# Optimization experiments

Hardware: AMD Instinct MI355X
Metric: run time of the kernel (lower is better)

Reference implementation:

```python
import jax, jax.numpy as jnp
import numpy as np

B, N, M, D = 128, 256, 8, 768  # batch, input patches, memory tokens, embed dim


def setup_inputs() -> dict:
    key = jax.random.key(0)
    ks = jax.random.split(key, 6)
    w_scale = D ** -0.5
    return {
        "x": jax.random.normal(ks[0], (B, N, D), dtype=jnp.float32),
        "memory": jax.random.normal(ks[1], (M, D), dtype=jnp.float32) * 0.02,
        "Wq": jax.random.normal(ks[2], (D, D), dtype=jnp.float32) * w_scale,
        "bq": jnp.zeros((D,), dtype=jnp.float32),
        "Wk": jax.random.normal(ks[3], (D, D), dtype=jnp.float32) * w_scale,
        "bk": jnp.zeros((D,), dtype=jnp.float32),
        "Wv": jax.random.normal(ks[4], (D, D), dtype=jnp.float32) * w_scale,
        "bv": jnp.zeros((D,), dtype=jnp.float32),
        "Wo": jax.random.normal(ks[5], (D, D), dtype=jnp.float32) * w_scale,
        "bo": jnp.zeros((D,), dtype=jnp.float32),
    }


def reference(x, memory, Wq, bq, Wk, bk, Wv, bv, Wo, bo):
    b, n, d = x.shape
    m = memory.shape[0]
    t = n + m
    scaling = d ** -0.5  # mha.scaling = 1/sqrt(input_dim)
    # concat input patches with expanded memory tokens: [B, T, D]
    cat = jnp.concatenate([x, jnp.broadcast_to(memory[None], (b, m, d))], axis=1)
    q = cat @ Wq + bq
    k = cat @ Wk + bk
    v = cat @ Wv + bv
    # full attention matrix [B, T, T], softmax over keys
    att = jax.nn.softmax(jnp.einsum("bqd,bkd->bqk", q, k) * scaling, axis=-1)
    # post-softmax multiplicative mask: zero all rows for memory-token queries
    row_mask = (jnp.arange(t) < n).astype(att.dtype)[None, :, None]  # [1, T, 1]
    att = att * row_mask
    head_out = jnp.einsum("bqk,bkd->bqd", att, v)
    attended = head_out @ Wo + bo
    # return only the input-patch part (split(...)[0])
    return attended[:, :n, :]
```

## Files before the change

kernel.cpp:

```cpp
#include <hip/hip_runtime.h>
#include <hip/hip_bf16.h>

typedef __attribute__((ext_vector_type(4))) float f32x4;
typedef __attribute__((ext_vector_type(8))) short short8;
typedef __attribute__((ext_vector_type(4))) unsigned short us4;
typedef unsigned short u16;

#define DEVI __device__ __forceinline__

#define BB 128
#define NN 256
#define MMEM 8
#define DD 768
#define TT 264
#define TP 320
#define SP 384
#define AROWS2 33024

DEVI u16 f2bf(float f) {
  __hip_bfloat16 b = __float2bfloat16(f);
  u16 u; __builtin_memcpy(&u, &b, 2); return u;
}

DEVI float bf2f(u16 u) {
  unsigned int v = ((unsigned int)u) << 16;
  float f; __builtin_memcpy(&f, &v, 4); return f;
}

DEVI void gload_lds16(const void* g, void* l) {
  __builtin_amdgcn_global_load_lds((const __attribute__((address_space(1))) void*)g,
                                   (__attribute__((address_space(3))) void*)l, 16, 0, 0);
}


__global__ __launch_bounds__(256)
void conv_x(const float* __restrict__ x, const float* __restrict__ mem, u16* __restrict__ Ab) {
  const long total4 = (long)AROWS2 * DD / 4;
  for (long i = (long)blockIdx.x * blockDim.x + threadIdx.x; i < total4;
       i += (long)gridDim.x * blockDim.x) {
    long e = i * 4;
    int row = (int)(e / DD);
    int cb  = (int)(e % DD);
    f32x4 v = {0.f, 0.f, 0.f, 0.f};
    if (row < BB * NN)             v = *(const f32x4*)(x   + (size_t)row * DD + cb);
    else if (row < BB * NN + MMEM) v = *(const f32x4*)(mem + (size_t)(row - BB * NN) * DD + cb);
    us4 o = {f2bf(v[0]), f2bf(v[1]), f2bf(v[2]), f2bf(v[3])};
    *(us4*)(Ab + e) = o;
  }
}

__global__ __launch_bounds__(256)
void conv_w(const float* __restrict__ Wq, const float* __restrict__ Wk,
            const float* __restrict__ Wv, const float* __restrict__ Wo,
            u16* __restrict__ Wqt, u16* __restrict__ Wkt,
            u16* __restrict__ Wvt, u16* __restrict__ Wot) {
  const int total = 4 * DD * DD;
  for (int i = blockIdx.x * blockDim.x + threadIdx.x; i < total;
       i += gridDim.x * blockDim.x) {
    int mat = i / (DD * DD), rem = i % (DD * DD);
    int j = rem / DD, d = rem % DD;
    const float* W = (mat == 0) ? Wq : (mat == 1) ? Wk : (mat == 2) ? Wv : Wo;
    u16* Wt = (mat == 0) ? Wqt : (mat == 1) ? Wkt : (mat == 2) ? Wvt : Wot;
    Wt[(size_t)j * DD + d] = f2bf(W[(size_t)d * DD + j]);
  }
}


#define BAR()    __builtin_amdgcn_s_barrier()
#define CFENCE() asm volatile("" ::: "memory")
#define VM2()    asm volatile("s_waitcnt vmcnt(2)" ::: "memory")
#define VMW0()   asm volatile("s_waitcnt vmcnt(0)" ::: "memory")

#define STG(gb, ld, isB, ss, rg, kt) do {                                       \
    const u16* _s = (gb) + (size_t)((rg) * 16 + srow) * (ld) + (kt) * 64 + scol;\
    char* _d = smem + (ss) * 65536 + (isB) * 32768 + (rg) * 2048;               \
    gload_lds16(_s, _d);                                                        \
    gload_lds16(_s + 32, _d + 1024);                                            \
  } while (0)

#define STG_A0(ss, kt) STG(Ab, LDA, 0, ss, ((w & 3) | ((w & 4) << 1)), kt)
#define STG_B0(ss, kt) STG(Bb, LDB, 1, ss, ((w & 1) | ((w & 6) << 1)), kt)
#define STG_A1(ss, kt) STG(Ab, LDA, 0, ss, (((w & 3) | ((w & 4) << 1)) + 4), kt)
#define STG_B1(ss, kt) STG(Bb, LDB, 1, ss, (((w & 1) | ((w & 6) << 1)) + 2), kt)

#define RD_A(dst, s, QM)                                                          \
  _Pragma("unroll") for (int mi = 0; mi < 4; ++mi)                                \
  _Pragma("unroll") for (int ks = 0; ks < 2; ++ks)                                \
    dst[mi][ks] = *(const short8*)(smem + (s) * 65536 +                           \
                    ((wm * 8 + (QM) * 4 + mi) * 2 + ks) * 1024 + fbase);

#define RD_B(dst, s, QN)                                                          \
  _Pragma("unroll") for (int ni = 0; ni < 2; ++ni)                                \
  _Pragma("unroll") for (int ks = 0; ks < 2; ++ks)                                \
    dst[ni][ks] = *(const short8*)(smem + (s) * 65536 + 32768 +                   \
                    ((wn * 4 + (QN) * 2 + ni) * 2 + ks) * 1024 + fbase);

#define MM(FA, FB, QM, QN)                                                        \
  _Pragma("unroll") for (int mi = 0; mi < 4; ++mi)                                \
  _Pragma("unroll") for (int ni = 0; ni < 2; ++ni)                                \
  _Pragma("unroll") for (int ks = 0; ks < 2; ++ks)                                \
    acc[(QM)*4+mi][(QN)*2+ni] = __builtin_amdgcn_mfma_f32_16x16x32_bf16(          \
        FA[mi][ks], FB[ni][ks], acc[(QM)*4+mi][(QN)*2+ni], 0, 0, 0);

template<int MODE>
__global__ __launch_bounds__(512)
void gemm256(const u16* __restrict__ A, const u16* __restrict__ Bq,
             const u16* __restrict__ Bk, const u16* __restrict__ Bv,
             const float* __restrict__ b0, const float* __restrict__ b1,
             const float* __restrict__ b2,
             u16* __restrict__ Oq, u16* __restrict__ Ok, u16* __restrict__ Ov,
             float* __restrict__ FO, int NT)
{
  extern __shared__ char smem[];
  const int tid = threadIdx.x;
  const int l = tid & 63;
  const int w = tid >> 6;
  const int wm = w >> 2, wn = w & 3;

  constexpr int LDA = (MODE == 2) ? TP : DD;
  constexpr int LDB = (MODE == 2) ? TP : DD;

  const int nwg = gridDim.x * gridDim.y;
  const int lin = blockIdx.y * gridDim.x + blockIdx.x;
  const int qq = nwg >> 3, rr = nwg & 7;
  const int xcd = lin & 7, idx = lin >> 3;
  const int wg = (xcd < rr ? xcd * (qq + 1) : rr * (qq + 1) + (xcd - rr) * qq) + idx;
  const int tn = wg % gridDim.x;
  const int tmz = wg / gridDim.x;

  const u16* Ab; const u16* Bb;
  int matsel = 0;
  if constexpr (MODE == 0) {
    Ab = A + (size_t)tmz * 256 * DD;
    matsel = tn / 3;
    const u16* Wp = (matsel == 0) ? Bq : (matsel == 1) ? Bk : Bv;
    Bb = Wp + (size_t)(tn % 3) * 256 * DD;
  } else if constexpr (MODE == 1) {
    Ab = A + (size_t)tmz * 256 * DD;
    Bb = Bq + (size_t)tn * 256 * DD;
  } else {
    Ab = A + (size_t)tmz * NN * TP;
    Bb = Bq + ((size_t)tmz * DD + tn * 256) * TP;
  }

  const int jj = (l < 32) ? l : (l ^ 2);
  const int srow = jj >> 2;
  const int scol = (jj & 3) * 8;
  const int fbase = (((l & 15) * 64) + ((l >> 4) * 16)) ^ (((l >> 3) & 1) << 5);

  f32x4 acc[8][4];
  #pragma unroll
  for (int i = 0; i < 8; ++i)
    #pragma unroll
    for (int jx = 0; jx < 4; ++jx) acc[i][jx] = (f32x4){0.f, 0.f, 0.f, 0.f};

  short8 fa0[4][2], fa1[4][2], fb0[2][2], fb1[2][2];

  STG_A0(0, 0); STG_B0(0, 0); STG_A1(0, 0); STG_B1(0, 0);
  VMW0(); BAR(); CFENCE();
  RD_A(fa0, 0, 0); RD_B(fb0, 0, 0);

  for (int g = 0; g < NT; ++g) {
    const int s = g & 1, ss = s ^ 1;
    const int st = (g + 1 < NT) ? (g + 1) : (NT - 1);

    VM2(); BAR(); CFENCE();
    RD_A(fa1, s, 1);
    STG_A0(ss, st);
    __builtin_amdgcn_s_setprio(1); MM(fa0, fb0, 0, 0); __builtin_amdgcn_s_setprio(0);

    VM2(); BAR(); CFENCE();
    RD_B(fb1, s, 1);
    STG_B0(ss, st);
    __builtin_amdgcn_s_setprio(1); MM(fa1, fb0, 1, 0); __builtin_amdgcn_s_setprio(0);

    STG_A1(ss, st);
    __builtin_amdgcn_s_setprio(1); MM(fa0, fb1, 0, 1); __builtin_amdgcn_s_setprio(0);

    VM2(); BAR(); CFENCE();
    RD_A(fa0, ss, 0); RD_B(fb0, ss, 0);
    STG_B1(ss, st);
    __builtin_amdgcn_s_setprio(1); MM(fa1, fb1, 1, 1); __builtin_amdgcn_s_setprio(0);
  }

  const int fr = l & 15, fro = (l >> 4) * 4;
  if constexpr (MODE == 0) {
    const float* bias = (matsel == 0) ? b0 : (matsel == 1) ? b1 : b2;
    u16* ob = (matsel == 0) ? Oq : (matsel == 1) ? Ok : Ov;
    const int cb = (tn % 3) * 256 + wn * 64;
    const size_t rb = (size_t)tmz * 256 + wm * 128;
    #pragma unroll
    for (int MI = 0; MI < 8; ++MI)
      #pragma unroll
      for (int NI = 0; NI < 4; ++NI) {
        const int col = cb + NI * 16 + fr;
        const float bvv = bias[col];
        #pragma unroll
        for (int r = 0; r < 4; ++r)
          ob[(rb + MI * 16 + fro + r) * DD + col] = f2bf(acc[MI][NI][r] + bvv);
      }
  } else if constexpr (MODE == 1) {
    const int cb = tn * 256 + wn * 64;
    const size_t rb = (size_t)tmz * 256 + wm * 128;
    #pragma unroll
    for (int MI = 0; MI < 8; ++MI)
      #pragma unroll
      for (int NI = 0; NI < 4; ++NI) {
        const int col = cb + NI * 16 + fr;
        const float bvv = b0[col];
        #pragma unroll
        for (int r = 0; r < 4; ++r)
          FO[(rb + MI * 16 + fro + r) * DD + col] = acc[MI][NI][r] + bvv;
      }
  } else {
    const int cb = tn * 256 + wn * 64;
    const size_t rb = (size_t)tmz * NN + wm * 128;
    #pragma unroll
    for (int MI = 0; MI < 8; ++MI)
      #pragma unroll
      for (int NI = 0; NI < 4; ++NI) {
        const int col = cb + NI * 16 + fr;
        #pragma unroll
        for (int r = 0; r < 4; ++r)
          Oq[(rb + MI * 16 + fro + r) * DD + col] = f2bf(acc[MI][NI][r]);
      }
  }
}


__global__ __launch_bounds__(256)
void gemm_s(const u16* __restrict__ A, const u16* __restrict__ Bm,
            u16* __restrict__ F0)
{
  const int tid = threadIdx.x;
  const int l  = tid & 63;
  const int w  = tid >> 6;
  const int wm = w >> 1, wn = w & 1;
  const int tm = blockIdx.x, tn = blockIdx.y, z = blockIdx.z;

  __shared__ u16 lsA[128 * 32];
  __shared__ u16 lsB[128 * 32];

  const u16* Abase = A + ((size_t)z * NN + tm * 128) * DD;

  f32x4 acc[4][4];
  #pragma unroll
  for (int i = 0; i < 4; i++)
    #pragma unroll
    for (int j = 0; j < 4; j++) acc[i][j] = (f32x4){0.f, 0.f, 0.f, 0.f};

  const int srow = l >> 2;
  const int scol = (l & 3) * 8;

  for (int kt = 0; kt < 24; ++kt) {
    const int kpos = kt * 32 + scol;
    #pragma unroll
    for (int q = 0; q < 2; ++q) {
      const int r = q * 64 + w * 16 + srow;
      gload_lds16(Abase + (size_t)r * DD + kpos, &lsA[q * 2048 + w * 512]);
    }
    #pragma unroll
    for (int q = 0; q < 2; ++q) {
      const int r = q * 64 + w * 16 + srow;
      const int t = tn * 128 + r;
      const int rr = (t < NN) ? (z * NN + t)
                   : ((t < TT) ? (BB * NN + t - NN) : BB * NN);
      gload_lds16(Bm + (size_t)rr * DD + kpos, &lsB[q * 2048 + w * 512]);
    }
    __syncthreads();

    const int fr = l & 15, fk = (l >> 4) * 8;
    short8 fa[4], fb[4];
    #pragma unroll
    for (int mi = 0; mi < 4; mi++)
      fa[mi] = *(const short8*)&lsA[(wm * 64 + mi * 16 + fr) * 32 + fk];
    #pragma unroll
    for (int ni = 0; ni < 4; ni++)
      fb[ni] = *(const short8*)&lsB[(wn * 64 + ni * 16 + fr) * 32 + fk];
    #pragma unroll
    for (int mi = 0; mi < 4; mi++)
      #pragma unroll
      for (int ni = 0; ni < 4; ni++)
        acc[mi][ni] = __builtin_amdgcn_mfma_f32_16x16x32_bf16(fa[mi], fb[ni], acc[mi][ni], 0, 0, 0);
    __syncthreads();
  }

  const int fr  = l & 15;
  const int fro = (l >> 4) * 4;
  const float scl = 0.03608439182435161f;
  u16* Sb = F0 + (size_t)z * NN * SP;
  const int cb = tn * 128 + wn * 64;
  const int rb = tm * 128 + wm * 64;
  #pragma unroll
  for (int mi = 0; mi < 4; mi++)
    #pragma unroll
    for (int ni = 0; ni < 4; ni++)
      #pragma unroll
      for (int r = 0; r < 4; r++)
        Sb[(size_t)(rb + mi * 16 + fro + r) * SP + cb + ni * 16 + fr] = f2bf(acc[mi][ni][r] * scl);
}


__global__ __launch_bounds__(256)
void softmax_k(const u16* __restrict__ S, u16* __restrict__ P) {
  const int l = threadIdx.x & 63;
  const int row = blockIdx.x * 4 + (threadIdx.x >> 6);
  const u16* s = S + (size_t)row * SP;
  float v0 = bf2f(s[l]), v1 = bf2f(s[64 + l]), v2 = bf2f(s[128 + l]), v3 = bf2f(s[192 + l]);
  float v4 = (l < 8) ? bf2f(s[256 + l]) : -__builtin_inff();
  float m = fmaxf(fmaxf(fmaxf(v0, v1), fmaxf(v2, v3)), v4);
  #pragma unroll
  for (int off = 32; off; off >>= 1) m = fmaxf(m, __shfl_xor(m, off));
  float e0 = __expf(v0 - m), e1 = __expf(v1 - m), e2 = __expf(v2 - m), e3 = __expf(v3 - m);
  float e4 = (l < 8) ? __expf(v4 - m) : 0.f;
  float sum = e0 + e1 + e2 + e3 + e4;
  #pragma unroll
  for (int off = 32; off; off >>= 1) sum += __shfl_xor(sum, off);
  const float inv = 1.f / sum;
  u16* p = P + (size_t)row * TP;
  p[l] = f2bf(e0 * inv); p[64 + l] = f2bf(e1 * inv);
  p[128 + l] = f2bf(e2 * inv); p[192 + l] = f2bf(e3 * inv);
  if (l < 8) p[256 + l] = f2bf(e4 * inv);
  else       p[256 + l] = 0;
}


__global__ __launch_bounds__(256)
void transpose_v(const u16* __restrict__ V, u16* __restrict__ Vt) {
  __shared__ u16 ls[64 * 66];
  const int b = blockIdx.z;
  const int d0 = blockIdx.x * 64;
  const int t0 = blockIdx.y * 64;
  const int tid = threadIdx.x;
  #pragma unroll
  for (int q = 0; q < 2; ++q) {
    const int idx = q * 256 + tid;
    const int tr = idx >> 3;
    const int dg = (idx & 7) * 8;
    const int t = t0 + tr;
    short8 v = (short8)(short)0;
    if (t < NN)       v = *(const short8*)(V + ((size_t)b * NN + t) * DD + d0 + dg);
    else if (t < TT)  v = *(const short8*)(V + (size_t)(BB * NN + t - NN) * DD + d0 + dg);
    #pragma unroll
    for (int e = 0; e < 8; ++e) ls[tr * 66 + dg + e] = (u16)v[e];
  }
  __syncthreads();
  #pragma unroll
  for (int q = 0; q < 2; ++q) {
    const int idx = q * 256 + tid;
    const int dr = idx >> 3;
    const int tg = (idx & 7) * 8;
    short8 v;
    #pragma unroll
    for (int e = 0; e < 8; ++e) v[e] = (short)ls[(tg + e) * 66 + dr];
    *(short8*)(Vt + ((size_t)b * DD + d0 + dr) * TP + t0 + tg) = v;
  }
}


extern "C" void kernel_launch(void* const* d_in, const int* in_sizes, int n_in,
                              void* d_out, int out_size, void* d_ws, size_t ws_size,
                              hipStream_t stream) {
  const float* x   = (const float*)d_in[0];
  const float* mem = (const float*)d_in[1];
  const float* Wq  = (const float*)d_in[2];
  const float* bq  = (const float*)d_in[3];
  const float* Wk  = (const float*)d_in[4];
  const float* bk  = (const float*)d_in[5];
  const float* Wv  = (const float*)d_in[6];
  const float* bv  = (const float*)d_in[7];
  const float* Wo  = (const float*)d_in[8];
  const float* bo  = (const float*)d_in[9];
  float* out = (float*)d_out;
  (void)ws_size; (void)in_sizes; (void)n_in; (void)out_size;

  const size_t QKV_B = (size_t)AROWS2 * DD * 2;
  char* wsb = (char*)d_ws;
  u16* Qb  = (u16*)(wsb);
  u16* Kb  = (u16*)(wsb + QKV_B);
  u16* Vb  = (u16*)(wsb + 2 * QKV_B);
  u16* Vt  = (u16*)(wsb);
  u16* O   = (u16*)(wsb + (size_t)BB * DD * TP * 2);
  u16* Wot = (u16*)(wsb + 3 * QKV_B);

  u16*   Ab  = (u16*)d_out;
  u16*   S   = (u16*)d_out;
  u16*   P   = (u16*)((char*)d_out + QKV_B);
  u16*   Wqt = (u16*)((char*)d_out + 97124352);
  u16*   Wkt = Wqt + (size_t)DD * DD;
  u16*   Wvt = Wkt + (size_t)DD * DD;

  conv_x<<<2048, 256, 0, stream>>>(x, mem, Ab);
  conv_w<<<1024, 256, 0, stream>>>(Wq, Wk, Wv, Wo, Wqt, Wkt, Wvt, Wot);

  gemm256<0><<<dim3(9, 129), 512, 131072, stream>>>(
      Ab, Wqt, Wkt, Wvt, bq, bk, bv, Qb, Kb, Vb, nullptr, 12);

  gemm_s<<<dim3(2, 3, BB), 256, 0, stream>>>(Qb, Kb, S);

  softmax_k<<<8192, 256, 0, stream>>>(S, P);

  transpose_v<<<dim3(12, 5, BB), 256, 0, stream>>>(Vb, Vt);

  gemm256<2><<<dim3(3, 128), 512, 131072, stream>>>(
      P, Vt, nullptr, nullptr, nullptr, nullptr, nullptr,
      O, nullptr, nullptr, nullptr, 5);

  gemm256<1><<<dim3(3, 128), 512, 131072, stream>>>(
      O, Wot, nullptr, nullptr, bo, nullptr, nullptr,
      nullptr, nullptr, nullptr, out, 12);
}
```

Before: 330.5 us.

## Double-buffer and software-pipeline the score GEMM with swizzled LDS and setprio

Rewrites the S=QK^T GEMM main loop to use K-tiles of 64 with two LDS stages, interleaving global-to-LDS prefetch of the next tile with MFMA compute on quadrant fragments of the current tile. LDS reads use an XOR-swizzled layout to avoid bank conflicts, and MFMA blocks are wrapped in s_setprio to favor compute issue. The aim is to hide global memory latency and cut the two barriers per iteration. In exchange it uses 64KB of LDS, which lowers occupancy, and depends on careful vmcnt waits whose correctness is hard to verify.

```diff
diff --git a/kernel.cpp b/kernel.cpp
--- a/kernel.cpp
+++ b/kernel.cpp
@@ -228,61 +228,95 @@
 }
 
 
+#define SSTG_A(ss, rg, kt) do {                                                  \
+    const u16* _s = Abase + (size_t)((rg) * 16 + srow) * DD + (kt) * 64 + scol;  \
+    char* _d = smem_s + (ss) * 32768 + (rg) * 2048;                              \
+    gload_lds16(_s, _d);                                                         \
+    gload_lds16(_s + 32, _d + 1024);                                             \
+  } while (0)
+
+#define SSTG_B(ss, rg, kt) do {                                                  \
+    const int t_ = tn * 128 + (rg) * 16 + srow;                                  \
+    const int rr_ = (t_ < NN) ? (z * NN + t_)                                    \
+                  : ((t_ < TT) ? (BB * NN + t_ - NN) : BB * NN);                 \
+    const u16* _s = Bm + (size_t)rr_ * DD + (kt) * 64 + scol;                    \
+    char* _d = smem_s + (ss) * 32768 + 16384 + (rg) * 2048;                      \
+    gload_lds16(_s, _d);                                                         \
+    gload_lds16(_s + 32, _d + 1024);                                             \
+  } while (0)
+
+#define SRD_A(dst, s, QM)                                                         \
+  _Pragma("unroll") for (int mi = 0; mi < 2; ++mi)                                \
+  _Pragma("unroll") for (int ks = 0; ks < 2; ++ks)                                \
+    dst[mi][ks] = *(const short8*)(smem_s + (s) * 32768 +                         \
+                    ((wm * 4 + (QM) * 2 + mi) * 2 + ks) * 1024 + fbase);
+
+#define SRD_B(dst, s, QN)                                                         \
+  _Pragma("unroll") for (int ni = 0; ni < 2; ++ni)                                \
+  _Pragma("unroll") for (int ks = 0; ks < 2; ++ks)                                \
+    dst[ni][ks] = *(const short8*)(smem_s + (s) * 32768 + 16384 +                 \
+                    ((wn * 4 + (QN) * 2 + ni) * 2 + ks) * 1024 + fbase);
+
+#define SMM(FA, FB, QM, QN)                                                       \
+  _Pragma("unroll") for (int mi = 0; mi < 2; ++mi)                                \
+  _Pragma("unroll") for (int ni = 0; ni < 2; ++ni)                                \
+  _Pragma("unroll") for (int ks = 0; ks < 2; ++ks)                                \
+    acc[(QM)*2+mi][(QN)*2+ni] = __builtin_amdgcn_mfma_f32_16x16x32_bf16(          \
+        FA[mi][ks], FB[ni][ks], acc[(QM)*2+mi][(QN)*2+ni], 0, 0, 0);
+
 __global__ __launch_bounds__(256)
 void gemm_s(const u16* __restrict__ A, const u16* __restrict__ Bm,
             u16* __restrict__ F0)
 {
+  __shared__ char smem_s[65536];
   const int tid = threadIdx.x;
   const int l  = tid & 63;
   const int w  = tid >> 6;
   const int wm = w >> 1, wn = w & 1;
   const int tm = blockIdx.x, tn = blockIdx.y, z = blockIdx.z;
 
-  __shared__ u16 lsA[128 * 32];
-  __shared__ u16 lsB[128 * 32];
-
   const u16* Abase = A + ((size_t)z * NN + tm * 128) * DD;
 
+  const int jj = (l < 32) ? l : (l ^ 2);
+  const int srow = jj >> 2;
+  const int scol = (jj & 3) * 8;
+  const int fbase = (((l & 15) * 64) + ((l >> 4) * 16)) ^ (((l >> 3) & 1) << 5);
+
+  const int rg0 = (w & 1) | ((w & 2) << 1);
+
   f32x4 acc[4][4];
   #pragma unroll
   for (int i = 0; i < 4; i++)
     #pragma unroll
     for (int j = 0; j < 4; j++) acc[i][j] = (f32x4){0.f, 0.f, 0.f, 0.f};
 
-  const int srow = l >> 2;
-  const int scol = (l & 3) * 8;
-
-  for (int kt = 0; kt < 24; ++kt) {
-    const int kpos = kt * 32 + scol;
-    #pragma unroll
-    for (int q = 0; q < 2; ++q) {
-      const int r = q * 64 + w * 16 + srow;
-      gload_lds16(Abase + (size_t)r * DD + kpos, &lsA[q * 2048 + w * 512]);
-    }
-    #pragma unroll
-    for (int q = 0; q < 2; ++q) {
-      const int r = q * 64 + w * 16 + srow;
-      const int t = tn * 128 + r;
-      const int rr = (t < NN) ? (z * NN + t)
-                   : ((t < TT) ? (BB * NN + t - NN) : BB * NN);
-      gload_lds16(Bm + (size_t)rr * DD + kpos, &lsB[q * 2048 + w * 512]);
-    }
-    __syncthreads();
-
-    const int fr = l & 15, fk = (l >> 4) * 8;
-    short8 fa[4], fb[4];
-    #pragma unroll
-    for (int mi = 0; mi < 4; mi++)
-      fa[mi] = *(const short8*)&lsA[(wm * 64 + mi * 16 + fr) * 32 + fk];
-    #pragma unroll
-    for (int ni = 0; ni < 4; ni++)
-      fb[ni] = *(const short8*)&lsB[(wn * 64 + ni * 16 + fr) * 32 + fk];
-    #pragma unroll
-    for (int mi = 0; mi < 4; mi++)
-      #pragma unroll
-      for (int ni = 0; ni < 4; ni++)
-        acc[mi][ni] = __builtin_amdgcn_mfma_f32_16x16x32_bf16(fa[mi], fb[ni], acc[mi][ni], 0, 0, 0);
-    __syncthreads();
+  short8 fa0[2][2], fa1[2][2], fb0[2][2], fb1[2][2];
+
+  SSTG_A(0, rg0, 0); SSTG_B(0, rg0, 0); SSTG_A(0, rg0 + 2, 0); SSTG_B(0, rg0 + 2, 0);
+  VMW0(); BAR(); CFENCE();
+  SRD_A(fa0, 0, 0); SRD_B(fb0, 0, 0);
+
+  for (int g = 0; g < 12; ++g) {
+    const int s = g & 1, ss = s ^ 1;
+    const int st = (g + 1 < 12) ? (g + 1) : 11;
+
+    VM2(); BAR(); CFENCE();
+    SRD_A(fa1, s, 1);
+    SSTG_A(ss, rg0, st);
+    __builtin_amdgcn_s_setprio(1); SMM(fa0, fb0, 0, 0); __builtin_amdgcn_s_setprio(0);
+
+    VM2(); BAR(); CFENCE();
+    SRD_B(fb1, s, 1);
+    SSTG_B(ss, rg0, st);
+    __builtin_amdgcn_s_setprio(1); SMM(fa1, fb0, 1, 0); __builtin_amdgcn_s_setprio(0);
+
+    SSTG_A(ss, rg0 + 2, st);
+    __builtin_amdgcn_s_setprio(1); SMM(fa0, fb1, 0, 1); __builtin_amdgcn_s_setprio(0);
+
+    VM2(); BAR(); CFENCE();
+    SRD_A(fa0, ss, 0); SRD_B(fb0, ss, 0);
+    SSTG_B(ss, rg0 + 2, st);
+    __builtin_amdgcn_s_setprio(1); SMM(fa1, fb1, 1, 1); __builtin_amdgcn_s_setprio(0);
   }
 
   const int fr  = l & 15;
```

Measured after the change: 325.7 us, median of 2. About the same (-1.4%).
